# Performance work log

Hardware: AMD Instinct MI355X
Metric: run time of the kernel (lower is better)

The kernel has to match this reference:

```python
import jax, jax.numpy as jnp
import numpy as np

T, B, C = 1024, 8, 1024
H, K, P = 16, 7, 3  # num_heads, kernel_size, padding_l
R = C // H


def setup_inputs() -> dict:
    key = jax.random.key(0)
    k1, k2, k3, k4 = jax.random.split(key, 4)
    x = jax.random.normal(k1, (T, B, C), dtype=jnp.float32)
    # weight_linear: Linear(C -> H*K) with bias
    lim = 1.0 / np.sqrt(C)
    W_lin = jax.random.uniform(k2, (H * K, C), minval=-lim, maxval=lim, dtype=jnp.float32)
    b_lin = jax.random.uniform(k3, (H * K,), minval=-lim, maxval=lim, dtype=jnp.float32)
    conv_bias = jnp.zeros((C,), dtype=jnp.float32)
    return {"x": x, "W_lin": W_lin, "b_lin": b_lin, "conv_bias": conv_bias}


def reference(x, W_lin, b_lin, conv_bias):
    # per-position dynamic filters: (T, B, H*K)
    w = jnp.einsum('tbc,oc->tbo', x, W_lin) + b_lin
    # weight_softmax=True, renorm_padding=False: softmax over kernel dim
    w = jax.nn.softmax(w.reshape(T * B * H, K), axis=-1)
    # (T, B*H, K) -> (B*H, T, K)
    w = w.reshape(T, B * H, K).transpose(1, 0, 2)
    # x as (B*H, T, R)
    xv = x.reshape(T, B * H, R).transpose(1, 0, 2)
    # band-matrix bmm == sliding window: out[t] = sum_k w[t,k] * x[t - P + k]
    x_pad = jnp.pad(xv, ((0, 0), (P, K - 1 - P), (0, 0)))
    windows = jnp.stack([x_pad[:, k:k + T] for k in range(K)], axis=2)  # (BH, T, K, R)
    out = jnp.einsum('btk,btkr->btr', w, windows)  # (BH, T, R)
    out = out.transpose(1, 0, 2).reshape(T, B, C)
    return out + conv_bias[None, None, :]
```

## Files before the change

kernel.cpp:

```cpp
#include <hip/hip_runtime.h>
#include <stdint.h>

#define T_DIM 1024
#define B_DIM 8
#define C_DIM 1024
#define H_DIM 16
#define K_SZ  7
#define P_PAD 3
#define O_DIM (H_DIM * K_SZ)
#define TB    (T_DIM * B_DIM)

typedef __attribute__((ext_vector_type(8))) short bf16x8;
typedef __attribute__((ext_vector_type(4))) float f32x4;
typedef __attribute__((ext_vector_type(4))) uint32_t u32x4;

union FragU { uint32_t u[4]; bf16x8 v; };

__device__ inline uint32_t pk_bf16(float a, float b) {
  uint32_t ua = __float_as_uint(a), ub = __float_as_uint(b);
  ua += 0x7FFFu + ((ua >> 16) & 1u);
  ub += 0x7FFFu + ((ub >> 16) & 1u);
  return (ua >> 16) | (ub & 0xFFFF0000u);
}

__device__ inline bf16x8 load_bf16x8_cvt(const float* __restrict__ p) {
  float4 lo = *reinterpret_cast<const float4*>(p);
  float4 hi = *reinterpret_cast<const float4*>(p + 4);
  FragU f;
  f.u[0] = pk_bf16(lo.x, lo.y);
  f.u[1] = pk_bf16(lo.z, lo.w);
  f.u[2] = pk_bf16(hi.x, hi.y);
  f.u[3] = pk_bf16(hi.z, hi.w);
  return f.v;
}

__global__ __launch_bounds__(256) void prep_wfrag_kernel(
    const float* __restrict__ Wl, uint16_t* __restrict__ Wf) {
  const int t  = blockIdx.x * 256 + threadIdx.x;
  const int f  = t >> 6;
  const int l  = t & 63;
  const int ks = f / 7;
  const int nf = f - ks * 7;
  const int row = nf * 16 + (l & 15);
  const int kb  = ks * 32 + (l >> 4) * 8;
  bf16x8 v = load_bf16x8_cvt(Wl + (size_t)row * C_DIM + kb);
  *reinterpret_cast<bf16x8*>(Wf + (size_t)t * 8) = v;
}

template <bool PREPPED>
__global__ __launch_bounds__(256) void fused_dynconv_kernel(
    const float* __restrict__ x, const float* __restrict__ Wl,
    const uint16_t* __restrict__ Wf, const float* __restrict__ bl,
    const float* __restrict__ cb, float* __restrict__ out) {
  __shared__ char  xbf[22 * 2048];
  __shared__ float part[16][116];
  __shared__ float wsm[16][17][8];

  const int tid  = threadIdx.x;
  const int wv   = tid >> 6;
  const int lane = tid & 63;
  const int l15  = lane & 15;
  const int oct  = lane >> 4;

  const int bid    = blockIdx.x;
  const int w8     = bid >> 3;
  const int t_tile = (bid & 7) * 8 + (w8 & 7);
  const int b      = w8 >> 3;
  const int t0     = t_tile * 16;

  {
#pragma unroll
    for (int it = 0; it < 11; ++it) {
      const int task = tid + it * 256;
      const int q    = task >> 7;
      const int c16  = task & 127;
      const int trow = min(max(t0 + q - P_PAD, 0), T_DIM - 1);
      const float* __restrict__ src =
          x + ((size_t)(trow * B_DIM + b)) * C_DIM + c16 * 8;
      float4 v0 = *reinterpret_cast<const float4*>(src);
      float4 v1 = *reinterpret_cast<const float4*>(src + 4);
      FragU f;
      f.u[0] = pk_bf16(v0.x, v0.y);
      f.u[1] = pk_bf16(v0.z, v0.w);
      f.u[2] = pk_bf16(v1.x, v1.y);
      f.u[3] = pk_bf16(v1.z, v1.w);
      const int dst = q * 2048 + ((c16 * 16) ^ ((q & 7) << 4));
      *reinterpret_cast<bf16x8*>(xbf + dst) = f.v;
    }
  }
  __syncthreads();

  {
    const int nf0 = wv * 2;
    const int nfc = (wv == 3) ? 1 : 2;
    f32x4 acc0 = (f32x4)(0.f), acc1 = (f32x4)(0.f);
    const int arow  = 3 + l15;
    const int abase = arow * 2048;
    const int axor  = (arow & 7) << 4;
#pragma unroll
    for (int ks = 0; ks < 32; ++ks) {
      bf16x8 a = *reinterpret_cast<const bf16x8*>(
          xbf + abase + ((ks * 64 + oct * 16) ^ axor));
      bf16x8 b0, b1;
      if (PREPPED) {
        b0 = *reinterpret_cast<const bf16x8*>(
            Wf + ((size_t)((ks * 7 + nf0) * 64) + lane) * 8);
        if (nfc == 2)
          b1 = *reinterpret_cast<const bf16x8*>(
              Wf + ((size_t)((ks * 7 + nf0 + 1) * 64) + lane) * 8);
      } else {
        b0 = load_bf16x8_cvt(Wl + (size_t)(nf0 * 16 + l15) * C_DIM + ks * 32 + oct * 8);
        if (nfc == 2)
          b1 = load_bf16x8_cvt(Wl + (size_t)((nf0 + 1) * 16 + l15) * C_DIM + ks * 32 + oct * 8);
      }
      acc0 = __builtin_amdgcn_mfma_f32_16x16x32_bf16(a, b0, acc0, 0, 0, 0);
      if (nfc == 2)
        acc1 = __builtin_amdgcn_mfma_f32_16x16x32_bf16(a, b1, acc1, 0, 0, 0);
    }
#pragma unroll
    for (int r = 0; r < 4; ++r)
      part[oct * 4 + r][nf0 * 16 + l15] = acc0[r];
    if (nfc == 2) {
#pragma unroll
      for (int r = 0; r < 4; ++r)
        part[oct * 4 + r][(nf0 + 1) * 16 + l15] = acc1[r];
    }
  }
  __syncthreads();

  {
    const int row = tid >> 4;
    const int h   = tid & 15;
    float lg[7];
    float m = -1e30f;
#pragma unroll
    for (int j = 0; j < 7; ++j) {
      float s_ = part[row][h * 7 + j] + bl[h * 7 + j];
      lg[j] = s_;
      m = fmaxf(m, s_);
    }
    float s = 0.f;
#pragma unroll
    for (int j = 0; j < 7; ++j) { lg[j] = __expf(lg[j] - m); s += lg[j]; }
    const float inv = 1.0f / s;
#pragma unroll
    for (int j = 0; j < 7; ++j) wsm[row][h][j] = lg[j] * inv;
  }
  __syncthreads();

  {
    const int row   = tid >> 4;
    const int t15   = tid & 15;
    const int tglob = t0 + row;
    float okf[7];
#pragma unroll
    for (int j = 0; j < 7; ++j) {
      int tp = tglob + j - P_PAD;
      okf[j] = (tp >= 0 && tp < T_DIM) ? 1.f : 0.f;
    }
    float* __restrict__ obase = out + ((size_t)(tglob * B_DIM + b)) * C_DIM;

#pragma unroll
    for (int ii = 0; ii < 8; ++ii) {
      const int ch0  = ii * 128 + t15 * 8;
      const int head = ii * 2 + (t15 >> 3);
      float4 w0 = *reinterpret_cast<const float4*>(&wsm[row][head][0]);
      float4 w1 = *reinterpret_cast<const float4*>(&wsm[row][head][4]);
      const float wj[7] = {w0.x, w0.y, w0.z, w0.w, w1.x, w1.y, w1.z};
      float4 c0 = *reinterpret_cast<const float4*>(cb + ch0);
      float4 c1 = *reinterpret_cast<const float4*>(cb + ch0 + 4);
      float a0 = c0.x, a1 = c0.y, a2 = c0.z, a3 = c0.w;
      float a4 = c1.x, a5 = c1.y, a6 = c1.z, a7 = c1.w;
#pragma unroll
      for (int j = 0; j < 7; ++j) {
        const float w = wj[j] * okf[j];
        const int q = row + j;
        const u32x4 d = *reinterpret_cast<const u32x4*>(
            xbf + q * 2048 + ((ii * 256 + t15 * 16) ^ ((q & 7) << 4)));
        a0 += w * __uint_as_float(d.x << 16);
        a1 += w * __uint_as_float(d.x & 0xffff0000u);
        a2 += w * __uint_as_float(d.y << 16);
        a3 += w * __uint_as_float(d.y & 0xffff0000u);
        a4 += w * __uint_as_float(d.z << 16);
        a5 += w * __uint_as_float(d.z & 0xffff0000u);
        a6 += w * __uint_as_float(d.w << 16);
        a7 += w * __uint_as_float(d.w & 0xffff0000u);
      }
      *reinterpret_cast<float4*>(obase + ch0)     = make_float4(a0, a1, a2, a3);
      *reinterpret_cast<float4*>(obase + ch0 + 4) = make_float4(a4, a5, a6, a7);
    }
  }
}

extern "C" void kernel_launch(void* const* d_in, const int* in_sizes, int n_in,
                              void* d_out, int out_size, void* d_ws, size_t ws_size,
                              hipStream_t stream) {
  const float* x  = (const float*)d_in[0];
  const float* Wl = (const float*)d_in[1];
  const float* bl = (const float*)d_in[2];
  const float* cb = (const float*)d_in[3];
  float* out = (float*)d_out;

  const bool prepped = ws_size >= 262144;

  if (prepped) {
    uint16_t* wf = (uint16_t*)d_ws;
    prep_wfrag_kernel<<<(32 * 7 * 64) / 256, 256, 0, stream>>>(Wl, wf);
    fused_dynconv_kernel<true><<<TB / 16, 256, 0, stream>>>(x, Wl, wf, bl, cb, out);
  } else {
    fused_dynconv_kernel<false><<<TB / 16, 256, 0, stream>>>(x, Wl, nullptr, bl, cb, out);
  }
}
```

Baseline: 33.25 us.

## Double block size to 512 threads with split-K GEMM and wider conv phase

Doubles the threads per block from 256 to 512. The filter-logit GEMM is split along K across two wave groups, and the softmax sums their partial results from a doubled shared buffer. The load and convolution phases spread the same work over more threads, with 32 threads per row instead of 16. The aim is more parallelism and latency hiding per block for the same tile. The cost is an idle half of the block during the softmax and possibly lower occupancy from register pressure.

After: 30.21 us. -9.1%, faster.

```diff
diff --git a/kernel.cpp b/kernel.cpp
--- a/kernel.cpp
+++ b/kernel.cpp
@@ -48,12 +48,12 @@
 }
 
 template <bool PREPPED>
-__global__ __launch_bounds__(256) void fused_dynconv_kernel(
+__global__ __launch_bounds__(512) void fused_dynconv_kernel(
     const float* __restrict__ x, const float* __restrict__ Wl,
     const uint16_t* __restrict__ Wf, const float* __restrict__ bl,
     const float* __restrict__ cb, float* __restrict__ out) {
   __shared__ char  xbf[22 * 2048];
-  __shared__ float part[16][116];
+  __shared__ float part[2][16][116];
   __shared__ float wsm[16][17][8];
 
   const int tid  = threadIdx.x;
@@ -70,48 +70,53 @@
 
   {
 #pragma unroll
-    for (int it = 0; it < 11; ++it) {
-      const int task = tid + it * 256;
-      const int q    = task >> 7;
-      const int c16  = task & 127;
-      const int trow = min(max(t0 + q - P_PAD, 0), T_DIM - 1);
-      const float* __restrict__ src =
-          x + ((size_t)(trow * B_DIM + b)) * C_DIM + c16 * 8;
-      float4 v0 = *reinterpret_cast<const float4*>(src);
-      float4 v1 = *reinterpret_cast<const float4*>(src + 4);
-      FragU f;
-      f.u[0] = pk_bf16(v0.x, v0.y);
-      f.u[1] = pk_bf16(v0.z, v0.w);
-      f.u[2] = pk_bf16(v1.x, v1.y);
-      f.u[3] = pk_bf16(v1.z, v1.w);
-      const int dst = q * 2048 + ((c16 * 16) ^ ((q & 7) << 4));
-      *reinterpret_cast<bf16x8*>(xbf + dst) = f.v;
+    for (int it = 0; it < 6; ++it) {
+      const int task = tid + it * 512;
+      if (task < 22 * 128) {
+        const int q    = task >> 7;
+        const int c16  = task & 127;
+        const int trow = min(max(t0 + q - P_PAD, 0), T_DIM - 1);
+        const float* __restrict__ src =
+            x + ((size_t)(trow * B_DIM + b)) * C_DIM + c16 * 8;
+        float4 v0 = *reinterpret_cast<const float4*>(src);
+        float4 v1 = *reinterpret_cast<const float4*>(src + 4);
+        FragU f;
+        f.u[0] = pk_bf16(v0.x, v0.y);
+        f.u[1] = pk_bf16(v0.z, v0.w);
+        f.u[2] = pk_bf16(v1.x, v1.y);
+        f.u[3] = pk_bf16(v1.z, v1.w);
+        const int dst = q * 2048 + ((c16 * 16) ^ ((q & 7) << 4));
+        *reinterpret_cast<bf16x8*>(xbf + dst) = f.v;
+      }
     }
   }
   __syncthreads();
 
   {
-    const int nf0 = wv * 2;
-    const int nfc = (wv == 3) ? 1 : 2;
+    const int kh  = wv >> 2;
+    const int nfq = wv & 3;
+    const int nf0 = nfq * 2;
+    const int nfc = (nfq == 3) ? 1 : 2;
     f32x4 acc0 = (f32x4)(0.f), acc1 = (f32x4)(0.f);
     const int arow  = 3 + l15;
     const int abase = arow * 2048;
     const int axor  = (arow & 7) << 4;
 #pragma unroll
-    for (int ks = 0; ks < 32; ++ks) {
+    for (int s = 0; s < 16; ++s) {
+      const int ksg = kh * 16 + s;
       bf16x8 a = *reinterpret_cast<const bf16x8*>(
-          xbf + abase + ((ks * 64 + oct * 16) ^ axor));
+          xbf + abase + ((ksg * 64 + oct * 16) ^ axor));
       bf16x8 b0, b1;
       if (PREPPED) {
         b0 = *reinterpret_cast<const bf16x8*>(
-            Wf + ((size_t)((ks * 7 + nf0) * 64) + lane) * 8);
+            Wf + ((size_t)((ksg * 7 + nf0) * 64) + lane) * 8);
         if (nfc == 2)
           b1 = *reinterpret_cast<const bf16x8*>(
-              Wf + ((size_t)((ks * 7 + nf0 + 1) * 64) + lane) * 8);
+              Wf + ((size_t)((ksg * 7 + nf0 + 1) * 64) + lane) * 8);
       } else {
-        b0 = load_bf16x8_cvt(Wl + (size_t)(nf0 * 16 + l15) * C_DIM + ks * 32 + oct * 8);
+        b0 = load_bf16x8_cvt(Wl + (size_t)(nf0 * 16 + l15) * C_DIM + ksg * 32 + oct * 8);
         if (nfc == 2)
-          b1 = load_bf16x8_cvt(Wl + (size_t)((nf0 + 1) * 16 + l15) * C_DIM + ks * 32 + oct * 8);
+          b1 = load_bf16x8_cvt(Wl + (size_t)((nf0 + 1) * 16 + l15) * C_DIM + ksg * 32 + oct * 8);
       }
       acc0 = __builtin_amdgcn_mfma_f32_16x16x32_bf16(a, b0, acc0, 0, 0, 0);
       if (nfc == 2)
@@ -119,23 +124,24 @@
     }
 #pragma unroll
     for (int r = 0; r < 4; ++r)
-      part[oct * 4 + r][nf0 * 16 + l15] = acc0[r];
+      part[kh][oct * 4 + r][nf0 * 16 + l15] = acc0[r];
     if (nfc == 2) {
 #pragma unroll
       for (int r = 0; r < 4; ++r)
-        part[oct * 4 + r][(nf0 + 1) * 16 + l15] = acc1[r];
+        part[kh][oct * 4 + r][(nf0 + 1) * 16 + l15] = acc1[r];
     }
   }
   __syncthreads();
 
-  {
+  if (tid < 256) {
     const int row = tid >> 4;
     const int h   = tid & 15;
     float lg[7];
     float m = -1e30f;
 #pragma unroll
     for (int j = 0; j < 7; ++j) {
-      float s_ = part[row][h * 7 + j] + bl[h * 7 + j];
+      const int c = h * 7 + j;
+      float s_ = part[0][row][c] + part[1][row][c] + bl[c];
       lg[j] = s_;
       m = fmaxf(m, s_);
     }
@@ -149,8 +155,8 @@
   __syncthreads();
 
   {
-    const int row   = tid >> 4;
-    const int t15   = tid & 15;
+    const int row   = tid >> 5;
+    const int t32   = tid & 31;
     const int tglob = t0 + row;
     float okf[7];
 #pragma unroll
@@ -161,9 +167,9 @@
     float* __restrict__ obase = out + ((size_t)(tglob * B_DIM + b)) * C_DIM;
 
 #pragma unroll
-    for (int ii = 0; ii < 8; ++ii) {
-      const int ch0  = ii * 128 + t15 * 8;
-      const int head = ii * 2 + (t15 >> 3);
+    for (int ii = 0; ii < 4; ++ii) {
+      const int ch0  = ii * 256 + t32 * 8;
+      const int head = ch0 >> 6;
       float4 w0 = *reinterpret_cast<const float4*>(&wsm[row][head][0]);
       float4 w1 = *reinterpret_cast<const float4*>(&wsm[row][head][4]);
       const float wj[7] = {w0.x, w0.y, w0.z, w0.w, w1.x, w1.y, w1.z};
@@ -176,7 +182,7 @@
         const float w = wj[j] * okf[j];
         const int q = row + j;
         const u32x4 d = *reinterpret_cast<const u32x4*>(
-            xbf + q * 2048 + ((ii * 256 + t15 * 16) ^ ((q & 7) << 4)));
+            xbf + q * 2048 + ((ch0 * 2) ^ ((q & 7) << 4)));
         a0 += w * __uint_as_float(d.x << 16);
         a1 += w * __uint_as_float(d.x & 0xffff0000u);
         a2 += w * __uint_as_float(d.y << 16);
@@ -206,8 +212,8 @@
   if (prepped) {
     uint16_t* wf = (uint16_t*)d_ws;
     prep_wfrag_kernel<<<(32 * 7 * 64) / 256, 256, 0, stream>>>(Wl, wf);
-    fused_dynconv_kernel<true><<<TB / 16, 256, 0, stream>>>(x, Wl, wf, bl, cb, out);
+    fused_dynconv_kernel<true><<<TB / 16, 512, 0, stream>>>(x, Wl, wf, bl, cb, out);
   } else {
-    fused_dynconv_kernel<false><<<TB / 16, 256, 0, stream>>>(x, Wl, nullptr, bl, cb, out);
-  }
-}
+    fused_dynconv_kernel<false><<<TB / 16, 512, 0, stream>>>(x, Wl, nullptr, bl, cb, out);
+  }
+}
```

## Tile one timestep across all batches and read conv window from global fp32

Applied to the files above, without the earlier changes.

Each block now handles one timestep across all 8 batch rows instead of 16 timesteps for one batch. Only those 8 rows are staged to LDS as bf16, for the MFMA logit GEMM. The convolution reads its 7 neighbouring timesteps directly from global fp32 memory, which removes the 22-row halo staging and gives full-precision inputs to the conv. This trades a smaller LDS footprint and higher occupancy for roughly 7x redundant global/L2 reads of x, and half the MFMA rows are wasted because only 8 of 16 rows are valid.

Result: slower. 36.32 us (+9.2%).

```diff
diff --git a/kernel.cpp b/kernel.cpp
--- a/kernel.cpp
+++ b/kernel.cpp
@@ -10,9 +10,11 @@
 #define O_DIM (H_DIM * K_SZ)
 #define TB    (T_DIM * B_DIM)
 
+#define XSTRIDE 2064
+
 typedef __attribute__((ext_vector_type(8))) short bf16x8;
 typedef __attribute__((ext_vector_type(4))) float f32x4;
-typedef __attribute__((ext_vector_type(4))) uint32_t u32x4;
+typedef __attribute__((ext_vector_type(2))) uint32_t u32x2;
 
 union FragU { uint32_t u[4]; bf16x8 v; };
 
@@ -24,13 +26,13 @@
 }
 
 __device__ inline bf16x8 load_bf16x8_cvt(const float* __restrict__ p) {
-  float4 lo = *reinterpret_cast<const float4*>(p);
-  float4 hi = *reinterpret_cast<const float4*>(p + 4);
+  f32x4 lo = *reinterpret_cast<const f32x4*>(p);
+  f32x4 hi = *reinterpret_cast<const f32x4*>(p + 4);
   FragU f;
-  f.u[0] = pk_bf16(lo.x, lo.y);
-  f.u[1] = pk_bf16(lo.z, lo.w);
-  f.u[2] = pk_bf16(hi.x, hi.y);
-  f.u[3] = pk_bf16(hi.z, hi.w);
+  f.u[0] = pk_bf16(lo[0], lo[1]);
+  f.u[1] = pk_bf16(lo[2], lo[3]);
+  f.u[2] = pk_bf16(hi[0], hi[1]);
+  f.u[3] = pk_bf16(hi[2], hi[3]);
   return f.v;
 }
 
@@ -48,13 +50,13 @@
 }
 
 template <bool PREPPED>
-__global__ __launch_bounds__(256) void fused_dynconv_kernel(
+__global__ __launch_bounds__(256, 4) void fused8_kernel(
     const float* __restrict__ x, const float* __restrict__ Wl,
     const uint16_t* __restrict__ Wf, const float* __restrict__ bl,
     const float* __restrict__ cb, float* __restrict__ out) {
-  __shared__ char  xbf[22 * 2048];
-  __shared__ float part[16][116];
-  __shared__ float wsm[16][17][8];
+  __shared__ char  xbf[8 * XSTRIDE];
+  __shared__ float lg[8][116];
+  __shared__ float wsm[8][116];
 
   const int tid  = threadIdx.x;
   const int wv   = tid >> 6;
@@ -62,31 +64,18 @@
   const int l15  = lane & 15;
   const int oct  = lane >> 4;
 
-  const int bid    = blockIdx.x;
-  const int w8     = bid >> 3;
-  const int t_tile = (bid & 7) * 8 + (w8 & 7);
-  const int b      = w8 >> 3;
-  const int t0     = t_tile * 16;
+  const int bid = blockIdx.x;
+  const int t0  = (bid & 7) * 128 + (bid >> 3);
 
-  {
+  const float* __restrict__ xrow0 = x + (size_t)t0 * B_DIM * C_DIM;
+
 #pragma unroll
-    for (int it = 0; it < 11; ++it) {
-      const int task = tid + it * 256;
-      const int q    = task >> 7;
-      const int c16  = task & 127;
-      const int trow = min(max(t0 + q - P_PAD, 0), T_DIM - 1);
-      const float* __restrict__ src =
-          x + ((size_t)(trow * B_DIM + b)) * C_DIM + c16 * 8;
-      float4 v0 = *reinterpret_cast<const float4*>(src);
-      float4 v1 = *reinterpret_cast<const float4*>(src + 4);
-      FragU f;
-      f.u[0] = pk_bf16(v0.x, v0.y);
-      f.u[1] = pk_bf16(v0.z, v0.w);
-      f.u[2] = pk_bf16(v1.x, v1.y);
-      f.u[3] = pk_bf16(v1.z, v1.w);
-      const int dst = q * 2048 + ((c16 * 16) ^ ((q & 7) << 4));
-      *reinterpret_cast<bf16x8*>(xbf + dst) = f.v;
-    }
+  for (int it = 0; it < 8; ++it) {
+    f32x4 v = *reinterpret_cast<const f32x4*>(xrow0 + it * C_DIM + tid * 4);
+    u32x2 d;
+    d.x = pk_bf16(v[0], v[1]);
+    d.y = pk_bf16(v[2], v[3]);
+    *reinterpret_cast<u32x2*>(xbf + it * XSTRIDE + tid * 8) = d;
   }
   __syncthreads();
 
@@ -94,13 +83,10 @@
     const int nf0 = wv * 2;
     const int nfc = (wv == 3) ? 1 : 2;
     f32x4 acc0 = (f32x4)(0.f), acc1 = (f32x4)(0.f);
-    const int arow  = 3 + l15;
-    const int abase = arow * 2048;
-    const int axor  = (arow & 7) << 4;
+    const char* __restrict__ arow = xbf + (l15 & 7) * XSTRIDE;
 #pragma unroll
     for (int ks = 0; ks < 32; ++ks) {
-      bf16x8 a = *reinterpret_cast<const bf16x8*>(
-          xbf + abase + ((ks * 64 + oct * 16) ^ axor));
+      bf16x8 a = *reinterpret_cast<const bf16x8*>(arow + ks * 64 + oct * 16);
       bf16x8 b0, b1;
       if (PREPPED) {
         b0 = *reinterpret_cast<const bf16x8*>(
@@ -117,77 +103,65 @@
       if (nfc == 2)
         acc1 = __builtin_amdgcn_mfma_f32_16x16x32_bf16(a, b1, acc1, 0, 0, 0);
     }
+    if (oct < 2) {
 #pragma unroll
-    for (int r = 0; r < 4; ++r)
-      part[oct * 4 + r][nf0 * 16 + l15] = acc0[r];
-    if (nfc == 2) {
+      for (int rr = 0; rr < 4; ++rr)
+        lg[oct * 4 + rr][nf0 * 16 + l15] = acc0[rr];
+      if (nfc == 2) {
 #pragma unroll
-      for (int r = 0; r < 4; ++r)
-        part[oct * 4 + r][(nf0 + 1) * 16 + l15] = acc1[r];
+        for (int rr = 0; rr < 4; ++rr)
+          lg[oct * 4 + rr][(nf0 + 1) * 16 + l15] = acc1[rr];
+      }
     }
   }
   __syncthreads();
 
-  {
+  if (tid < 128) {
     const int row = tid >> 4;
     const int h   = tid & 15;
-    float lg[7];
+    float v[7];
     float m = -1e30f;
 #pragma unroll
     for (int j = 0; j < 7; ++j) {
-      float s_ = part[row][h * 7 + j] + bl[h * 7 + j];
-      lg[j] = s_;
+      float s_ = lg[row][h * 7 + j] + bl[h * 7 + j];
+      v[j] = s_;
       m = fmaxf(m, s_);
     }
     float s = 0.f;
 #pragma unroll
-    for (int j = 0; j < 7; ++j) { lg[j] = __expf(lg[j] - m); s += lg[j]; }
+    for (int j = 0; j < 7; ++j) { v[j] = __expf(v[j] - m); s += v[j]; }
     const float inv = 1.0f / s;
 #pragma unroll
-    for (int j = 0; j < 7; ++j) wsm[row][h][j] = lg[j] * inv;
+    for (int j = 0; j < 7; ++j) wsm[row][h * 7 + j] = v[j] * inv;
   }
   __syncthreads();
 
   {
-    const int row   = tid >> 4;
-    const int t15   = tid & 15;
-    const int tglob = t0 + row;
+    const int b    = tid >> 5;
+    const int l32  = tid & 31;
+    const int grow = t0 * B_DIM + b;
+    const float* __restrict__ tp[7];
     float okf[7];
 #pragma unroll
     for (int j = 0; j < 7; ++j) {
-      int tp = tglob + j - P_PAD;
-      okf[j] = (tp >= 0 && tp < T_DIM) ? 1.f : 0.f;
+      const int t_ = t0 + j - P_PAD;
+      okf[j] = (t_ >= 0 && t_ < T_DIM) ? 1.f : 0.f;
+      const int g = min(max(t_, 0), T_DIM - 1);
+      tp[j] = x + ((size_t)(g * B_DIM + b)) * C_DIM;
     }
-    float* __restrict__ obase = out + ((size_t)(tglob * B_DIM + b)) * C_DIM;
-
+    float* __restrict__ obase = out + (size_t)grow * C_DIM;
 #pragma unroll
-    for (int ii = 0; ii < 8; ++ii) {
-      const int ch0  = ii * 128 + t15 * 8;
-      const int head = ii * 2 + (t15 >> 3);
-      float4 w0 = *reinterpret_cast<const float4*>(&wsm[row][head][0]);
-      float4 w1 = *reinterpret_cast<const float4*>(&wsm[row][head][4]);
-      const float wj[7] = {w0.x, w0.y, w0.z, w0.w, w1.x, w1.y, w1.z};
-      float4 c0 = *reinterpret_cast<const float4*>(cb + ch0);
-      float4 c1 = *reinterpret_cast<const float4*>(cb + ch0 + 4);
-      float a0 = c0.x, a1 = c0.y, a2 = c0.z, a3 = c0.w;
-      float a4 = c1.x, a5 = c1.y, a6 = c1.z, a7 = c1.w;
+    for (int cc = 0; cc < 8; ++cc) {
+      const int ch   = l32 * 4 + cc * 128;
+      const int head = ch >> 6;
+      const float* __restrict__ wr = &wsm[b][head * 7];
+      f32x4 a = *reinterpret_cast<const f32x4*>(cb + ch);
 #pragma unroll
       for (int j = 0; j < 7; ++j) {
-        const float w = wj[j] * okf[j];
-        const int q = row + j;
-        const u32x4 d = *reinterpret_cast<const u32x4*>(
-            xbf + q * 2048 + ((ii * 256 + t15 * 16) ^ ((q & 7) << 4)));
-        a0 += w * __uint_as_float(d.x << 16);
-        a1 += w * __uint_as_float(d.x & 0xffff0000u);
-        a2 += w * __uint_as_float(d.y << 16);
-        a3 += w * __uint_as_float(d.y & 0xffff0000u);
-        a4 += w * __uint_as_float(d.z << 16);
-        a5 += w * __uint_as_float(d.z & 0xffff0000u);
-        a6 += w * __uint_as_float(d.w << 16);
-        a7 += w * __uint_as_float(d.w & 0xffff0000u);
+        f32x4 d = *reinterpret_cast<const f32x4*>(tp[j] + ch);
+        a += (wr[j] * okf[j]) * d;
       }
-      *reinterpret_cast<float4*>(obase + ch0)     = make_float4(a0, a1, a2, a3);
-      *reinterpret_cast<float4*>(obase + ch0 + 4) = make_float4(a4, a5, a6, a7);
+      *reinterpret_cast<f32x4*>(obase + ch) = a;
     }
   }
 }
@@ -206,8 +180,8 @@
   if (prepped) {
     uint16_t* wf = (uint16_t*)d_ws;
     prep_wfrag_kernel<<<(32 * 7 * 64) / 256, 256, 0, stream>>>(Wl, wf);
-    fused_dynconv_kernel<true><<<TB / 16, 256, 0, stream>>>(x, Wl, wf, bl, cb, out);
+    fused8_kernel<true><<<T_DIM, 256, 0, stream>>>(x, Wl, wf, bl, cb, out);
   } else {
-    fused_dynconv_kernel<false><<<TB / 16, 256, 0, stream>>>(x, Wl, nullptr, bl, cb, out);
+    fused8_kernel<false><<<T_DIM, 256, 0, stream>>>(x, Wl, nullptr, bl, cb, out);
   }
 }
```
